# Optimization experiments

Measured on AMD Instinct MI355X. Metric: run time of the kernel, lower is better.

Reference implementation:

```python
import jax, jax.numpy as jnp
import numpy as np
import math

N = 30000; N0 = 18000; N1 = 12000; R = 5; E = 600000
H = 128; HM = 128; C = 8
L1 = 20.0; L2 = 30.0
THRESH = 0.3; THRESH_C = 1e-3
T_INNER = 20; K_OUTER = 8
EPS = 1e-5


def setup_inputs() -> dict:
    key = jax.random.key(0)
    ks = jax.random.split(key, 16)
    def w(k, shape):  # kaiming-ish fan_in init
        return jax.random.normal(k, shape, jnp.float32) / np.sqrt(shape[0])
    return {
        "feat0": jax.random.normal(ks[0], (N0, 256), jnp.float32),
        "feat1": jax.random.normal(ks[1], (N1, 128), jnp.float32),
        "W0": w(ks[2], (256, H)), "b0": jnp.zeros((H,), jnp.float32),
        "W1": w(ks[3], (128, H)), "b1": jnp.zeros((H,), jnp.float32),
        "Wm1": w(ks[4], (H, HM)), "bm1": jnp.zeros((HM,), jnp.float32),
        "Wm2": w(ks[5], (HM, HM)), "bm2": jnp.zeros((HM,), jnp.float32),
        "Wout": w(ks[6], (HM, C)), "bout": jnp.zeros((C,), jnp.float32),
        "src": jax.random.randint(ks[7], (E,), 0, N, jnp.int32),
        "dst": jax.random.randint(ks[8], (E,), 0, N, jnp.int32),
        "rel": jax.random.randint(ks[9], (E,), 0, R, jnp.int32),
    }


def _layernorm(z):
    m = z.mean(-1, keepdims=True)
    v = z.var(-1, keepdims=True)
    return (z - m) / jnp.sqrt(v + EPS)


def _forward(feat0, feat1, W0, b0, W1, b1, Wm1, bm1, Wm2, bm2, Wout, bout, src, dst, rel):
    # transfer (transf_type==2): per-type linear -> concat -> 2-layer MLP w/ layernorm
    h = jnp.concatenate([feat0 @ W0 + b0, feat1 @ W1 + b1], axis=0)   # (N, H)
    z = jax.nn.relu(_layernorm(h @ Wm1 + bm1))
    h = z @ Wm2 + bm2                                                 # (N, HM)
    # per-node standardization (torch std is unbiased, ddof=1), nan -> 0
    mu = h.mean(1, keepdims=True)
    sd = h.std(1, ddof=1, keepdims=True)
    out0 = jnp.nan_to_num((h - mu) / sd)

    # per-relation row degrees of the vertically stacked adjacency (R*N, N)
    key_e = rel * N + src                                             # (E,)
    deg = jax.ops.segment_sum(jnp.ones(E, jnp.float32), key_e, num_segments=R * N)
    safe = jnp.maximum(deg, 1.0)
    vals = jnp.where(deg > 0, 1.0 / safe, 0.0)[key_e]                 # row-normalized A weights
    dinv = jnp.where(deg > 0, 1.0 / jnp.sqrt(safe), 0.0)              # D^{-1/2}
    edge_dinv = dinv[key_e] * dinv[rel * N + dst]                     # (E,)
    active = (deg > 0).astype(jnp.float32).reshape(R, N)              # (R, N)

    def tv(x):  # relational total variation tr(X^T L_r X)/N, L_r = I - D^-1/2 A_r D^-1/2
        node_term = active @ (x * x).sum(1)                           # (R,)
        edot = (x[src] * x[dst]).sum(1)                               # (E,)
        edge_term = jax.ops.segment_sum(edge_dinv * edot, rel, num_segments=R)
        return (node_term - edge_term) / N

    ratio = 2.0 * L2 / L1
    c_l1tr = jnp.abs(tv(out0)).sum()
    u0 = jnp.full((R,), 1.0 / R, jnp.float32)

    def mirror_descent(u, w, l1tr):
        fi = l1tr + ratio
        def step(carry, t):
            u, act = carry
            T_t = jnp.sqrt(2.0 * math.log(R) / (t * fi * fi))
            u_ta = u * jnp.exp(-T_t * (ratio * u + w))
            u_new = u_ta / u_ta.sum()
            diff = jnp.sqrt(((u - u_new) ** 2).sum())
            u = jnp.where(act, u_new, u)
            return (u, act & (diff >= THRESH_C)), None
        ts = jnp.arange(1, T_INNER + 1, dtype=jnp.float32)
        (u, _), _ = jax.lax.scan(step, (u, jnp.array(True)), ts)
        return u

    def outer(carry, _):
        x, u, act = carry
        w = tv(x)
        l1tr = jnp.abs(w).sum()
        u = jnp.where(act, mirror_descent(u, w, l1tr), u)
        still = act & (l1tr / c_l1tr >= THRESH)
        ew = u[rel] * vals                                            # (E,)
        msg = jax.ops.segment_sum(ew[:, None] * x[dst], src, num_segments=N)  # (N, HM)
        x = jnp.where(still, x / (1.0 + L1) + (L1 / (1.0 + L1)) * msg, x)
        return (x, u, still), None

    (x, u, _), _ = jax.lax.scan(outer, (out0, u0, jnp.array(True)), None, length=K_OUTER)
    logits = x @ Wout + bout
    return logits, x, u


def reference(feat0, feat1, W0, b0, W1, b1, Wm1, bm1, Wm2, bm2, Wout, bout, src, dst, rel):
    return _forward(feat0, feat1, W0, b0, W1, b1, Wm1, bm1, Wm2, bm2, Wout, bout, src, dst, rel)
```

## Files before the change

kernel.cpp:

```cpp
#include <hip/hip_runtime.h>
#include <cmath>

typedef unsigned short ushort_t;
typedef unsigned int uint_t;

#define N_TOT 30000
#define N0_   18000
#define R_    5
#define E_    600000
#define RN    (R_ * N_TOT)
#define NC_   (N_TOT * 8)
#define NX_   (N_TOT * 128)
#define SCAN_NB ((RN + 1023) / 1024)

typedef __attribute__((ext_vector_type(8))) short bf16x8;
typedef __attribute__((ext_vector_type(4))) float f32x4;

__device__ __forceinline__ ushort_t f2bf(float f) {
    uint_t u = __float_as_uint(f);
    uint_t r = (u + 0x7fffu + ((u >> 16) & 1u)) >> 16;
    return (ushort_t)r;
}
__device__ __forceinline__ float bflo(uint_t v) { return __uint_as_float(v << 16); }
__device__ __forceinline__ float bfhi(uint_t v) { return __uint_as_float(v & 0xffff0000u); }

__global__ void init_kernel(float* ug, int* act) {
    if (threadIdx.x < 5) ug[threadIdx.x] = 0.2f;
    if (threadIdx.x == 0) act[0] = 1;
}

__global__ __launch_bounds__(256) void cvtfeat_kernel(const float* __restrict__ in,
                                                      ushort_t* __restrict__ out,
                                                      int nelem)
{
    int i = (blockIdx.x * 256 + threadIdx.x) * 4;
    if (i >= nelem) return;
    const float4 v = *(const float4*)(in + i);
    ushort_t o0 = f2bf(v.x), o1 = f2bf(v.y), o2 = f2bf(v.z), o3 = f2bf(v.w);
    uint_t p0 = (uint_t)o0 | ((uint_t)o1 << 16);
    uint_t p1 = (uint_t)o2 | ((uint_t)o3 << 16);
    uint2* op = (uint2*)(out + i);
    *op = make_uint2(p0, p1);
}

__global__ __launch_bounds__(256) void cvtw_kernel(const float* __restrict__ W,
                                                   ushort_t* __restrict__ wt, int K)
{
    int idx = blockIdx.x * 256 + threadIdx.x;
    if (idx >= 128 * K) return;
    int j = idx / K, k = idx - j * K;
    wt[idx] = f2bf(W[k * 128 + j]);
}

__global__ __launch_bounds__(256) void mlp_mfma_kernel(
    const ushort_t* __restrict__ fb0, const ushort_t* __restrict__ fb1,
    const ushort_t* __restrict__ wt0, const ushort_t* __restrict__ wt1,
    const ushort_t* __restrict__ wtm1, const ushort_t* __restrict__ wtm2,
    const float* __restrict__ b0, const float* __restrict__ b1,
    const float* __restrict__ bm1, const float* __restrict__ bm2,
    float* __restrict__ xout, ushort_t* __restrict__ xh)
{
    const int t = threadIdx.x;
    const int lane = t & 63;
    const int wv = t >> 6;
    const int lr = lane & 15;
    const int lg = lane >> 4;
    const int row0 = blockIdx.x * 32;

    __shared__ ushort_t hls[32][136];
    __shared__ float    tls[32][132];
    __shared__ ushort_t zls[32][136];

    #pragma unroll
    for (int mt = 0; mt < 2; ++mt) {
        const int rb = row0 + mt * 16;
        const bool is0 = (rb < N0_);
        const int r = min(rb + lr, N_TOT - 1);
        const ushort_t* __restrict__ fa =
            is0 ? fb0 + (size_t)r * 256 : fb1 + (size_t)(r - N0_) * 128;
        const ushort_t* __restrict__ wt = is0 ? wt0 : wt1;
        const int K = is0 ? 256 : 128;
        const int c0 = wv * 32 + lr;

        f32x4 a0 = {0.f, 0.f, 0.f, 0.f};
        f32x4 a1 = {0.f, 0.f, 0.f, 0.f};
        for (int ks = 0; ks < K; ks += 32) {
            const bf16x8 af = *(const bf16x8*)(fa + ks + lg * 8);
            const bf16x8 wb0 = *(const bf16x8*)(wt + (size_t)c0 * K + ks + lg * 8);
            const bf16x8 wb1 = *(const bf16x8*)(wt + (size_t)(c0 + 16) * K + ks + lg * 8);
            a0 = __builtin_amdgcn_mfma_f32_16x16x32_bf16(af, wb0, a0, 0, 0, 0);
            a1 = __builtin_amdgcn_mfma_f32_16x16x32_bf16(af, wb1, a1, 0, 0, 0);
        }
        const float bb0 = is0 ? b0[c0] : b1[c0];
        const float bb1 = is0 ? b0[c0 + 16] : b1[c0 + 16];
        #pragma unroll
        for (int j = 0; j < 4; ++j) {
            hls[mt * 16 + lg * 4 + j][c0]      = f2bf(a0[j] + bb0);
            hls[mt * 16 + lg * 4 + j][c0 + 16] = f2bf(a1[j] + bb1);
        }
    }
    __syncthreads();

    {
        const int c0 = wv * 32 + lr;
        f32x4 g00 = {0.f,0.f,0.f,0.f}, g01 = {0.f,0.f,0.f,0.f};
        f32x4 g10 = {0.f,0.f,0.f,0.f}, g11 = {0.f,0.f,0.f,0.f};
        for (int ks = 0; ks < 128; ks += 32) {
            const bf16x8 wb0 = *(const bf16x8*)(wtm1 + (size_t)c0 * 128 + ks + lg * 8);
            const bf16x8 wb1 = *(const bf16x8*)(wtm1 + (size_t)(c0 + 16) * 128 + ks + lg * 8);
            const bf16x8 af0 = *(const bf16x8*)(&hls[lr][ks + lg * 8]);
            const bf16x8 af1 = *(const bf16x8*)(&hls[16 + lr][ks + lg * 8]);
            g00 = __builtin_amdgcn_mfma_f32_16x16x32_bf16(af0, wb0, g00, 0, 0, 0);
            g01 = __builtin_amdgcn_mfma_f32_16x16x32_bf16(af0, wb1, g01, 0, 0, 0);
            g10 = __builtin_amdgcn_mfma_f32_16x16x32_bf16(af1, wb0, g10, 0, 0, 0);
            g11 = __builtin_amdgcn_mfma_f32_16x16x32_bf16(af1, wb1, g11, 0, 0, 0);
        }
        const float bb0 = bm1[c0], bb1 = bm1[c0 + 16];
        #pragma unroll
        for (int j = 0; j < 4; ++j) {
            tls[lg * 4 + j][c0]           = g00[j] + bb0;
            tls[lg * 4 + j][c0 + 16]      = g01[j] + bb1;
            tls[16 + lg * 4 + j][c0]      = g10[j] + bb0;
            tls[16 + lg * 4 + j][c0 + 16] = g11[j] + bb1;
        }
    }
    __syncthreads();

    {
        const int row = t >> 3, seg = t & 7;
        f32x4 v[4];
        float s = 0.f;
        #pragma unroll
        for (int i = 0; i < 4; ++i) {
            v[i] = *(const f32x4*)(&tls[row][seg * 16 + i * 4]);
            s += v[i][0] + v[i][1] + v[i][2] + v[i][3];
        }
        #pragma unroll
        for (int o = 1; o < 8; o <<= 1) s += __shfl_xor(s, o, 64);
        const float mean = s * (1.0f / 128.0f);
        float q = 0.f;
        #pragma unroll
        for (int i = 0; i < 4; ++i) {
            #pragma unroll
            for (int e = 0; e < 4; ++e) { float d = v[i][e] - mean; q = fmaf(d, d, q); }
        }
        #pragma unroll
        for (int o = 1; o < 8; o <<= 1) q += __shfl_xor(q, o, 64);
        const float inv = 1.0f / sqrtf(q * (1.0f / 128.0f) + 1e-5f);
        uint_t* zp = (uint_t*)&zls[row][0];
        #pragma unroll
        for (int i = 0; i < 4; ++i) {
            ushort_t z0 = f2bf(fmaxf((v[i][0] - mean) * inv, 0.0f));
            ushort_t z1 = f2bf(fmaxf((v[i][1] - mean) * inv, 0.0f));
            ushort_t z2 = f2bf(fmaxf((v[i][2] - mean) * inv, 0.0f));
            ushort_t z3 = f2bf(fmaxf((v[i][3] - mean) * inv, 0.0f));
            zp[(seg * 16 + i * 4) / 2]     = (uint_t)z0 | ((uint_t)z1 << 16);
            zp[(seg * 16 + i * 4) / 2 + 1] = (uint_t)z2 | ((uint_t)z3 << 16);
        }
    }
    __syncthreads();

    {
        const int c0 = wv * 32 + lr;
        f32x4 g00 = {0.f,0.f,0.f,0.f}, g01 = {0.f,0.f,0.f,0.f};
        f32x4 g10 = {0.f,0.f,0.f,0.f}, g11 = {0.f,0.f,0.f,0.f};
        for (int ks = 0; ks < 128; ks += 32) {
            const bf16x8 wb0 = *(const bf16x8*)(wtm2 + (size_t)c0 * 128 + ks + lg * 8);
            const bf16x8 wb1 = *(const bf16x8*)(wtm2 + (size_t)(c0 + 16) * 128 + ks + lg * 8);
            const bf16x8 af0 = *(const bf16x8*)(&zls[lr][ks + lg * 8]);
            const bf16x8 af1 = *(const bf16x8*)(&zls[16 + lr][ks + lg * 8]);
            g00 = __builtin_amdgcn_mfma_f32_16x16x32_bf16(af0, wb0, g00, 0, 0, 0);
            g01 = __builtin_amdgcn_mfma_f32_16x16x32_bf16(af0, wb1, g01, 0, 0, 0);
            g10 = __builtin_amdgcn_mfma_f32_16x16x32_bf16(af1, wb0, g10, 0, 0, 0);
            g11 = __builtin_amdgcn_mfma_f32_16x16x32_bf16(af1, wb1, g11, 0, 0, 0);
        }
        __syncthreads();
        const float bb0 = bm2[c0], bb1 = bm2[c0 + 16];
        #pragma unroll
        for (int j = 0; j < 4; ++j) {
            tls[lg * 4 + j][c0]           = g00[j] + bb0;
            tls[lg * 4 + j][c0 + 16]      = g01[j] + bb1;
            tls[16 + lg * 4 + j][c0]      = g10[j] + bb0;
            tls[16 + lg * 4 + j][c0 + 16] = g11[j] + bb1;
        }
    }
    __syncthreads();

    {
        const int row = t >> 3, seg = t & 7;
        const int n = row0 + row;
        f32x4 v[4];
        float s = 0.f;
        #pragma unroll
        for (int i = 0; i < 4; ++i) {
            v[i] = *(const f32x4*)(&tls[row][seg * 16 + i * 4]);
            s += v[i][0] + v[i][1] + v[i][2] + v[i][3];
        }
        #pragma unroll
        for (int o = 1; o < 8; o <<= 1) s += __shfl_xor(s, o, 64);
        const float mu = s * (1.0f / 128.0f);
        float q = 0.f;
        #pragma unroll
        for (int i = 0; i < 4; ++i) {
            #pragma unroll
            for (int e = 0; e < 4; ++e) { float d = v[i][e] - mu; q = fmaf(d, d, q); }
        }
        #pragma unroll
        for (int o = 1; o < 8; o <<= 1) q += __shfl_xor(q, o, 64);
        const float sd = sqrtf(q * (1.0f / 127.0f));
        const float inv = 1.0f / sd;
        if (n < N_TOT) {
            uint_t* xhp = (uint_t*)xh + (size_t)n * 64 + seg * 8;
            float* xop = xout + (size_t)n * 128 + seg * 16;
            #pragma unroll
            for (int i = 0; i < 4; ++i) {
                float rr[4];
                #pragma unroll
                for (int e = 0; e < 4; ++e) {
                    float r = (v[i][e] - mu) * inv;
                    if (!(fabsf(r) <= 3.402823466e38f)) {
                        r = (r != r) ? 0.0f : ((r > 0.0f) ? 3.402823466e38f : -3.402823466e38f);
                    }
                    rr[e] = r;
                }
                *(float4*)(xop + i * 4) = make_float4(rr[0], rr[1], rr[2], rr[3]);
                xhp[i * 2]     = (uint_t)f2bf(rr[0]) | ((uint_t)f2bf(rr[1]) << 16);
                xhp[i * 2 + 1] = (uint_t)f2bf(rr[2]) | ((uint_t)f2bf(rr[3]) << 16);
            }
        }
    }
}

__global__ void deg_kernel(const int* __restrict__ src, const int* __restrict__ rel,
                           int* __restrict__ deg_i)
{
    int e = blockIdx.x * 256 + threadIdx.x;
    if (e >= E_) return;
    atomicAdd(&deg_i[rel[e] * N_TOT + src[e]], 1);
}

__global__ void dinv_kernel(const int* __restrict__ deg_i, float* __restrict__ dinv)
{
    int i = blockIdx.x * 256 + threadIdx.x;
    if (i >= RN) return;
    int dg = deg_i[i];
    dinv[i] = (dg > 0) ? 1.0f / sqrtf((float)dg) : 0.0f;
}

__global__ __launch_bounds__(256) void scan1_kernel(const int* __restrict__ cnt,
                                                    int* __restrict__ rp,
                                                    int* __restrict__ bsum)
{
    __shared__ int wsum[4];
    const int t = threadIdx.x, lane = t & 63, w = t >> 6;
    const int i0 = blockIdx.x * 1024 + t * 4;
    const int v0 = (i0 + 0 < RN) ? cnt[i0 + 0] : 0;
    const int v1 = (i0 + 1 < RN) ? cnt[i0 + 1] : 0;
    const int v2 = (i0 + 2 < RN) ? cnt[i0 + 2] : 0;
    const int v3 = (i0 + 3 < RN) ? cnt[i0 + 3] : 0;
    const int s = v0 + v1 + v2 + v3;
    int sc = s;
    #pragma unroll
    for (int o = 1; o < 64; o <<= 1) { int tmp = __shfl_up(sc, o, 64); if (lane >= o) sc += tmp; }
    if (lane == 63) wsum[w] = sc;
    __syncthreads();
    int woff = 0;
    #pragma unroll
    for (int i = 0; i < 3; ++i) if (i < w) woff += wsum[i];
    int run = woff + sc - s;
    if (i0 + 0 < RN) rp[i0 + 0] = run; run += v0;
    if (i0 + 1 < RN) rp[i0 + 1] = run; run += v1;
    if (i0 + 2 < RN) rp[i0 + 2] = run; run += v2;
    if (i0 + 3 < RN) rp[i0 + 3] = run;
    if (t == 255) bsum[blockIdx.x] = woff + sc;
}

__global__ __launch_bounds__(256) void scan2_kernel(const int* __restrict__ bsum,
                                                    int* __restrict__ boff,
                                                    int* __restrict__ rp)
{
    __shared__ int wsum[4];
    const int t = threadIdx.x, lane = t & 63, w = t >> 6;
    const int v = (t < SCAN_NB) ? bsum[t] : 0;
    int sc = v;
    #pragma unroll
    for (int o = 1; o < 64; o <<= 1) { int tmp = __shfl_up(sc, o, 64); if (lane >= o) sc += tmp; }
    if (lane == 63) wsum[w] = sc;
    __syncthreads();
    int woff = 0;
    #pragma unroll
    for (int i = 0; i < 3; ++i) if (i < w) woff += wsum[i];
    boff[t] = woff + sc - v;
    if (t == 0) rp[RN] = E_;
}

__global__ __launch_bounds__(256) void scan3_kernel(int* __restrict__ rp,
                                                    const int* __restrict__ boff)
{
    const int off = boff[blockIdx.x];
    if (off == 0) return;
    const int i0 = blockIdx.x * 1024 + threadIdx.x * 4;
    if (i0 + 3 < RN) {
        int4* p = (int4*)(rp + i0);
        int4 q = *p;
        q.x += off; q.y += off; q.z += off; q.w += off;
        *p = q;
    } else {
        for (int i = 0; i < 4; ++i)
            if (i0 + i < RN) rp[i0 + i] += off;
    }
}

__global__ void scatter_kernel(const int* __restrict__ src, const int* __restrict__ dst,
                               const int* __restrict__ rel, const int* __restrict__ rp,
                               int* __restrict__ fill, const int* __restrict__ deg_i,
                               const float* __restrict__ dinv,
                               int* __restrict__ csr_dst, float* __restrict__ csr_w,
                               float* __restrict__ csr_edinv)
{
    int e = blockIdx.x * 256 + threadIdx.x;
    if (e >= E_) return;
    int s = src[e], r = rel[e], d = dst[e];
    int key = r * N_TOT + s;
    int pos = rp[key] + atomicAdd(&fill[key], 1);
    csr_dst[pos] = d;
    csr_w[pos] = 1.0f / (float)deg_i[key];
    csr_edinv[pos] = dinv[key] * dinv[r * N_TOT + d];
}

__global__ __launch_bounds__(256) void tv_kernel(
    const ushort_t* __restrict__ xh, const int* __restrict__ rp,
    const int* __restrict__ csr_dst, const float* __restrict__ csr_edinv,
    const int* __restrict__ act, int k, float* __restrict__ accbuf)
{
    if (act[k] == 0) return;
    const int lane = threadIdx.x & 63;
    const int wv = threadIdx.x >> 6;
    const int wid = blockIdx.x * 4 + wv;
    const int nw = gridDim.x * 4;
    float na[5] = {0, 0, 0, 0, 0};
    float ea[5] = {0, 0, 0, 0, 0};
    for (int n = wid; n < N_TOT; n += nw) {
        const uint_t vs = ((const uint_t*)(xh + (size_t)n * 128))[lane];
        const float sx = bflo(vs), sy = bfhi(vs);
        const float pp = fmaf(sx, sx, sy * sy);
        #pragma unroll
        for (int r = 0; r < 5; ++r) {
            const int e0 = rp[r * N_TOT + n];
            const int e1 = rp[r * N_TOT + n + 1];
            if (e1 > e0) na[r] += pp;
            float acc0 = 0.0f, acc1 = 0.0f;
            int e = e0;
            for (; e + 2 <= e1; e += 2) {
                const int dn0 = csr_dst[e];
                const int dn1 = csr_dst[e + 1];
                const float w0 = csr_edinv[e];
                const float w1 = csr_edinv[e + 1];
                const uint_t v0 = ((const uint_t*)(xh + (size_t)dn0 * 128))[lane];
                const uint_t v1 = ((const uint_t*)(xh + (size_t)dn1 * 128))[lane];
                acc0 = fmaf(w0, fmaf(sx, bflo(v0), sy * bfhi(v0)), acc0);
                acc1 = fmaf(w1, fmaf(sx, bflo(v1), sy * bfhi(v1)), acc1);
            }
            if (e < e1) {
                const int dn0 = csr_dst[e];
                const float w0 = csr_edinv[e];
                const uint_t v0 = ((const uint_t*)(xh + (size_t)dn0 * 128))[lane];
                acc0 = fmaf(w0, fmaf(sx, bflo(v0), sy * bfhi(v0)), acc0);
            }
            ea[r] += acc0 + acc1;
        }
    }
    __shared__ float sacc[4][10];
    #pragma unroll
    for (int r = 0; r < 5; ++r) {
        float a = na[r], b2 = ea[r];
        for (int o = 32; o > 0; o >>= 1) {
            a += __shfl_down(a, o, 64);
            b2 += __shfl_down(b2, o, 64);
        }
        if (lane == 0) { sacc[wv][r] = a; sacc[wv][5 + r] = b2; }
    }
    __syncthreads();
    if (threadIdx.x < 10) {
        float t = sacc[0][threadIdx.x] + sacc[1][threadIdx.x] +
                  sacc[2][threadIdx.x] + sacc[3][threadIdx.x];
        atomicAdd(&accbuf[k * 16 + threadIdx.x], t);
    }
}

__global__ void scalar_kernel(const float* __restrict__ accbuf, float* __restrict__ ug,
                              float* __restrict__ c_l1, int* __restrict__ act, int k)
{
    if (blockIdx.x != 0 || threadIdx.x >= 8) return;
    const int r = threadIdx.x;
    const int a = act[k];
    float w = (r < 5) ? (accbuf[k * 16 + r] - accbuf[k * 16 + 5 + r]) * (1.0f / 30000.0f)
                      : 0.0f;
    float l1 = fabsf(w);
    for (int o = 4; o > 0; o >>= 1) l1 += __shfl_xor(l1, o, 8);
    if (k == 0 && r == 0) c_l1[0] = l1;
    if (!a) { if (r == 0) act[k + 1] = 0; return; }
    float u = (r < 5) ? ug[r] : 0.0f;
    const float fi = l1 + 3.0f;
    bool mact = true;
    for (int t = 1; t <= 20; ++t) {
        float T = sqrtf(3.2188758248682006f / ((float)t * fi * fi));
        float ta = u * expf(-T * (3.0f * u + w));
        float ssum = ta;
        for (int o = 4; o > 0; o >>= 1) ssum += __shfl_xor(ssum, o, 8);
        float un = ta / ssum;
        float d0 = u - un;
        float dq = d0 * d0;
        for (int o = 4; o > 0; o >>= 1) dq += __shfl_xor(dq, o, 8);
        if (mact) u = un;
        mact = mact && (sqrtf(dq) >= 1e-3f);
    }
    if (r < 5) ug[r] = u;
    if (r == 0) act[k + 1] = (l1 / c_l1[0] >= 0.3f) ? 1 : 0;
}

__global__ __launch_bounds__(256) void msg_upd_kernel(
    float* __restrict__ x, const ushort_t* __restrict__ xh_in,
    ushort_t* __restrict__ xh_out,
    const int* __restrict__ rp, const int* __restrict__ csr_dst,
    const float* __restrict__ csr_w, const float* __restrict__ ug,
    const int* __restrict__ act, int k)
{
    if (act[k + 1] == 0) return;
    const int lane = threadIdx.x & 63;
    const int wid = blockIdx.x * 4 + (threadIdx.x >> 6);
    const int nw = gridDim.x * 4;
    const float u0 = ug[0], u1 = ug[1], u2 = ug[2], u3 = ug[3], u4 = ug[4];
    for (int n = wid; n < N_TOT; n += nw) {
        float ax0 = 0.0f, ay0 = 0.0f, ax1 = 0.0f, ay1 = 0.0f;
        #pragma unroll
        for (int r = 0; r < 5; ++r) {
            const float ur = (r == 0) ? u0 : (r == 1) ? u1 : (r == 2) ? u2 : (r == 3) ? u3 : u4;
            const int e0 = rp[r * N_TOT + n];
            const int e1 = rp[r * N_TOT + n + 1];
            int e = e0;
            for (; e + 2 <= e1; e += 2) {
                const float w0 = ur * csr_w[e];
                const float w1 = ur * csr_w[e + 1];
                const int dn0 = csr_dst[e];
                const int dn1 = csr_dst[e + 1];
                const uint_t v0 = ((const uint_t*)(xh_in + (size_t)dn0 * 128))[lane];
                const uint_t v1 = ((const uint_t*)(xh_in + (size_t)dn1 * 128))[lane];
                ax0 = fmaf(w0, bflo(v0), ax0);
                ay0 = fmaf(w0, bfhi(v0), ay0);
                ax1 = fmaf(w1, bflo(v1), ax1);
                ay1 = fmaf(w1, bfhi(v1), ay1);
            }
            if (e < e1) {
                const float w0 = ur * csr_w[e];
                const int dn0 = csr_dst[e];
                const uint_t v0 = ((const uint_t*)(xh_in + (size_t)dn0 * 128))[lane];
                ax0 = fmaf(w0, bflo(v0), ax0);
                ay0 = fmaf(w0, bfhi(v0), ay0);
            }
        }
        const float ci = 1.0f / 21.0f, cb = 20.0f / 21.0f;
        float2* xp = (float2*)(x + (size_t)n * 128);
        const float2 xs = xp[lane];
        const float nx_ = fmaf(cb, ax0 + ax1, xs.x * ci);
        const float ny_ = fmaf(cb, ay0 + ay1, xs.y * ci);
        xp[lane] = make_float2(nx_, ny_);
        ((uint_t*)(xh_out + (size_t)n * 128))[lane] =
            ((uint_t)f2bf(ny_) << 16) | (uint_t)f2bf(nx_);
    }
}

__global__ __launch_bounds__(256) void final_kernel(const float* __restrict__ x,
                                                    const float* __restrict__ Wout,
                                                    const float* __restrict__ bout,
                                                    const float* __restrict__ ug,
                                                    float* __restrict__ out)
{
    const int nl = threadIdx.x >> 7;
    const int n = blockIdx.x * 2 + nl;
    const int j = threadIdx.x & 127;
    const int lane = threadIdx.x & 63;
    const int wv = threadIdx.x >> 6;
    float xv = x[(size_t)n * 128 + j];
    out[(size_t)NC_ + (size_t)n * 128 + j] = xv;
    float p[8];
    #pragma unroll
    for (int c = 0; c < 8; ++c) p[c] = xv * Wout[j * 8 + c];
    #pragma unroll
    for (int c = 0; c < 8; ++c)
        for (int o = 32; o > 0; o >>= 1) p[c] += __shfl_down(p[c], o, 64);
    __shared__ float sp[4][8];
    if (lane == 0) {
        #pragma unroll
        for (int c = 0; c < 8; ++c) sp[wv][c] = p[c];
    }
    __syncthreads();
    if (j < 8) {
        int c = j;
        out[(size_t)n * 8 + c] = bout[c] + sp[2 * nl][c] + sp[2 * nl + 1][c];
    }
    if (blockIdx.x == 0 && threadIdx.x < 5)
        out[(size_t)NC_ + (size_t)NX_ + threadIdx.x] = ug[threadIdx.x];
}

extern "C" void kernel_launch(void* const* d_in, const int* in_sizes, int n_in,
                              void* d_out, int out_size, void* d_ws, size_t ws_size,
                              hipStream_t stream)
{
    const float* feat0 = (const float*)d_in[0];
    const float* feat1 = (const float*)d_in[1];
    const float* W0   = (const float*)d_in[2];
    const float* b0   = (const float*)d_in[3];
    const float* W1   = (const float*)d_in[4];
    const float* b1   = (const float*)d_in[5];
    const float* Wm1  = (const float*)d_in[6];
    const float* bm1  = (const float*)d_in[7];
    const float* Wm2  = (const float*)d_in[8];
    const float* bm2  = (const float*)d_in[9];
    const float* Wout = (const float*)d_in[10];
    const float* bout = (const float*)d_in[11];
    const int* src = (const int*)d_in[12];
    const int* dst = (const int*)d_in[13];
    const int* rel = (const int*)d_in[14];
    float* out = (float*)d_out;

    char* p = (char*)d_ws;
    auto alloc = [&](size_t bytes) { char* q = p; p += (bytes + 255) & ~(size_t)255; return q; };
    float*    xbuf      = (float*)   alloc((size_t)NX_ * 4);
    ushort_t* xh0       = (ushort_t*)alloc((size_t)NX_ * 2);
    ushort_t* xh1       = (ushort_t*)alloc((size_t)NX_ * 2);
    ushort_t* fb0       = (ushort_t*)alloc((size_t)N0_ * 256 * 2);
    ushort_t* fb1       = (ushort_t*)alloc((size_t)(N_TOT - N0_) * 128 * 2);
    ushort_t* wt0       = (ushort_t*)alloc((size_t)128 * 256 * 2);
    ushort_t* wt1       = (ushort_t*)alloc((size_t)128 * 128 * 2);
    ushort_t* wtm1      = (ushort_t*)alloc((size_t)128 * 128 * 2);
    ushort_t* wtm2      = (ushort_t*)alloc((size_t)128 * 128 * 2);
    int*      deg_i     = (int*)     alloc((size_t)RN * 4);
    float*    dinv      = (float*)   alloc((size_t)RN * 4);
    int*      rp        = (int*)     alloc(((size_t)RN + 1) * 4);
    int*      fill      = (int*)     alloc((size_t)RN * 4);
    int*      bsum      = (int*)     alloc((size_t)SCAN_NB * 4);
    int*      boff      = (int*)     alloc(256 * 4);
    int*      csr_dst   = (int*)     alloc((size_t)E_ * 4);
    float*    csr_w     = (float*)   alloc((size_t)E_ * 4);
    float*    csr_edinv = (float*)   alloc((size_t)E_ * 4);
    float*    accbuf    = (float*)   alloc(128 * 4);
    float*    ug        = (float*)   alloc(64);
    float*    c_l1      = (float*)   alloc(64);
    int*      act       = (int*)     alloc(64);

    hipMemsetAsync(deg_i, 0, (size_t)RN * 4, stream);
    hipMemsetAsync(fill, 0, (size_t)RN * 4, stream);
    hipMemsetAsync(accbuf, 0, 128 * 4, stream);
    init_kernel<<<1, 64, 0, stream>>>(ug, act);

    cvtfeat_kernel<<<(N0_ * 256 / 4 + 255) / 256, 256, 0, stream>>>(feat0, fb0, N0_ * 256);
    cvtfeat_kernel<<<((N_TOT - N0_) * 128 / 4 + 255) / 256, 256, 0, stream>>>(
        feat1, fb1, (N_TOT - N0_) * 128);
    cvtw_kernel<<<(128 * 256 + 255) / 256, 256, 0, stream>>>(W0, wt0, 256);
    cvtw_kernel<<<(128 * 128 + 255) / 256, 256, 0, stream>>>(W1, wt1, 128);
    cvtw_kernel<<<(128 * 128 + 255) / 256, 256, 0, stream>>>(Wm1, wtm1, 128);
    cvtw_kernel<<<(128 * 128 + 255) / 256, 256, 0, stream>>>(Wm2, wtm2, 128);

    mlp_mfma_kernel<<<(N_TOT + 31) / 32, 256, 0, stream>>>(
        fb0, fb1, wt0, wt1, wtm1, wtm2, b0, b1, bm1, bm2, xbuf, xh0);

    deg_kernel<<<(E_ + 255) / 256, 256, 0, stream>>>(src, rel, deg_i);
    dinv_kernel<<<(RN + 255) / 256, 256, 0, stream>>>(deg_i, dinv);
    scan1_kernel<<<SCAN_NB, 256, 0, stream>>>(deg_i, rp, bsum);
    scan2_kernel<<<1, 256, 0, stream>>>(bsum, boff, rp);
    scan3_kernel<<<SCAN_NB, 256, 0, stream>>>(rp, boff);
    scatter_kernel<<<(E_ + 255) / 256, 256, 0, stream>>>(src, dst, rel, rp, fill,
                                                         deg_i, dinv,
                                                         csr_dst, csr_w, csr_edinv);

    ushort_t* ha = xh0;
    ushort_t* hb = xh1;
    for (int k = 0; k < 8; ++k) {
        tv_kernel<<<2048, 256, 0, stream>>>(ha, rp, csr_dst, csr_edinv, act, k, accbuf);
        scalar_kernel<<<1, 64, 0, stream>>>(accbuf, ug, c_l1, act, k);
        msg_upd_kernel<<<2048, 256, 0, stream>>>(xbuf, ha, hb, rp, csr_dst, csr_w,
                                                 ug, act, k);
        ushort_t* t = ha; ha = hb; hb = t;
    }

    final_kernel<<<N_TOT / 2, 256, 0, stream>>>(xbuf, Wout, bout, ug, out);
}
```

Before: 470.9 us.

## Switch CSR to node-major relation layout and merge per-relation edge loops

Reorders the degree/row-pointer key from relation-major to node-major so each node's edges across all relations are contiguous. The TV and message-update kernels then walk one merged edge range per node, 4-way unrolled, and derive each edge's relation by comparing against the boundaries. Row pointers are read as wave-uniform scalars. This removes five short per-relation loops with remainder tails and raises in-flight gathers, at the cost of extra compare/select work per edge.

```diff
diff --git a/kernel.cpp b/kernel.cpp
--- a/kernel.cpp
+++ b/kernel.cpp
@@ -236,7 +236,7 @@
 {
     int e = blockIdx.x * 256 + threadIdx.x;
     if (e >= E_) return;
-    atomicAdd(&deg_i[rel[e] * N_TOT + src[e]], 1);
+    atomicAdd(&deg_i[src[e] * R_ + rel[e]], 1);
 }
 
 __global__ void dinv_kernel(const int* __restrict__ deg_i, float* __restrict__ dinv)
@@ -321,11 +321,11 @@
     int e = blockIdx.x * 256 + threadIdx.x;
     if (e >= E_) return;
     int s = src[e], r = rel[e], d = dst[e];
-    int key = r * N_TOT + s;
+    int key = s * R_ + r;
     int pos = rp[key] + atomicAdd(&fill[key], 1);
     csr_dst[pos] = d;
     csr_w[pos] = 1.0f / (float)deg_i[key];
-    csr_edinv[pos] = dinv[key] * dinv[r * N_TOT + d];
+    csr_edinv[pos] = dinv[key] * dinv[d * R_ + r];
 }
 
 __global__ __launch_bounds__(256) void tv_kernel(
@@ -341,44 +341,68 @@
     float na[5] = {0, 0, 0, 0, 0};
     float ea[5] = {0, 0, 0, 0, 0};
     for (int n = wid; n < N_TOT; n += nw) {
+        const int b0 = __builtin_amdgcn_readfirstlane(rp[n * R_ + 0]);
+        const int b1 = __builtin_amdgcn_readfirstlane(rp[n * R_ + 1]);
+        const int b2 = __builtin_amdgcn_readfirstlane(rp[n * R_ + 2]);
+        const int b3 = __builtin_amdgcn_readfirstlane(rp[n * R_ + 3]);
+        const int b4 = __builtin_amdgcn_readfirstlane(rp[n * R_ + 4]);
+        const int b5 = __builtin_amdgcn_readfirstlane(rp[n * R_ + 5]);
         const uint_t vs = ((const uint_t*)(xh + (size_t)n * 128))[lane];
         const float sx = bflo(vs), sy = bfhi(vs);
         const float pp = fmaf(sx, sx, sy * sy);
-        #pragma unroll
-        for (int r = 0; r < 5; ++r) {
-            const int e0 = rp[r * N_TOT + n];
-            const int e1 = rp[r * N_TOT + n + 1];
-            if (e1 > e0) na[r] += pp;
-            float acc0 = 0.0f, acc1 = 0.0f;
-            int e = e0;
-            for (; e + 2 <= e1; e += 2) {
-                const int dn0 = csr_dst[e];
-                const int dn1 = csr_dst[e + 1];
-                const float w0 = csr_edinv[e];
-                const float w1 = csr_edinv[e + 1];
-                const uint_t v0 = ((const uint_t*)(xh + (size_t)dn0 * 128))[lane];
-                const uint_t v1 = ((const uint_t*)(xh + (size_t)dn1 * 128))[lane];
-                acc0 = fmaf(w0, fmaf(sx, bflo(v0), sy * bfhi(v0)), acc0);
-                acc1 = fmaf(w1, fmaf(sx, bflo(v1), sy * bfhi(v1)), acc1);
+        if (b1 > b0) na[0] += pp;
+        if (b2 > b1) na[1] += pp;
+        if (b3 > b2) na[2] += pp;
+        if (b4 > b3) na[3] += pp;
+        if (b5 > b4) na[4] += pp;
+        int e = b0;
+        for (; e + 4 <= b5; e += 4) {
+            const int dn0 = csr_dst[e + 0];
+            const int dn1 = csr_dst[e + 1];
+            const int dn2 = csr_dst[e + 2];
+            const int dn3 = csr_dst[e + 3];
+            const float w0 = csr_edinv[e + 0];
+            const float w1 = csr_edinv[e + 1];
+            const float w2 = csr_edinv[e + 2];
+            const float w3 = csr_edinv[e + 3];
+            const uint_t v0 = ((const uint_t*)(xh + (size_t)dn0 * 128))[lane];
+            const uint_t v1 = ((const uint_t*)(xh + (size_t)dn1 * 128))[lane];
+            const uint_t v2 = ((const uint_t*)(xh + (size_t)dn2 * 128))[lane];
+            const uint_t v3 = ((const uint_t*)(xh + (size_t)dn3 * 128))[lane];
+            const float d0 = w0 * fmaf(sx, bflo(v0), sy * bfhi(v0));
+            const float d1 = w1 * fmaf(sx, bflo(v1), sy * bfhi(v1));
+            const float d2 = w2 * fmaf(sx, bflo(v2), sy * bfhi(v2));
+            const float d3 = w3 * fmaf(sx, bflo(v3), sy * bfhi(v3));
+            const int r0 = (e + 0 >= b1) + (e + 0 >= b2) + (e + 0 >= b3) + (e + 0 >= b4);
+            const int r1 = (e + 1 >= b1) + (e + 1 >= b2) + (e + 1 >= b3) + (e + 1 >= b4);
+            const int r2 = (e + 2 >= b1) + (e + 2 >= b2) + (e + 2 >= b3) + (e + 2 >= b4);
+            const int r3 = (e + 3 >= b1) + (e + 3 >= b2) + (e + 3 >= b3) + (e + 3 >= b4);
+            #pragma unroll
+            for (int rr = 0; rr < 5; ++rr) {
+                ea[rr] += (r0 == rr ? d0 : 0.0f) + (r1 == rr ? d1 : 0.0f) +
+                          (r2 == rr ? d2 : 0.0f) + (r3 == rr ? d3 : 0.0f);
             }
-            if (e < e1) {
-                const int dn0 = csr_dst[e];
-                const float w0 = csr_edinv[e];
-                const uint_t v0 = ((const uint_t*)(xh + (size_t)dn0 * 128))[lane];
-                acc0 = fmaf(w0, fmaf(sx, bflo(v0), sy * bfhi(v0)), acc0);
-            }
-            ea[r] += acc0 + acc1;
+        }
+        for (; e < b5; ++e) {
+            const int dn0 = csr_dst[e];
+            const float w0 = csr_edinv[e];
+            const uint_t v0 = ((const uint_t*)(xh + (size_t)dn0 * 128))[lane];
+            const float d0 = w0 * fmaf(sx, bflo(v0), sy * bfhi(v0));
+            const int r0 = (e >= b1) + (e >= b2) + (e >= b3) + (e >= b4);
+            #pragma unroll
+            for (int rr = 0; rr < 5; ++rr)
+                ea[rr] += (r0 == rr ? d0 : 0.0f);
         }
     }
     __shared__ float sacc[4][10];
     #pragma unroll
     for (int r = 0; r < 5; ++r) {
-        float a = na[r], b2 = ea[r];
+        float a = na[r], b = ea[r];
         for (int o = 32; o > 0; o >>= 1) {
             a += __shfl_down(a, o, 64);
-            b2 += __shfl_down(b2, o, 64);
-        }
-        if (lane == 0) { sacc[wv][r] = a; sacc[wv][5 + r] = b2; }
+            b += __shfl_down(b, o, 64);
+        }
+        if (lane == 0) { sacc[wv][r] = a; sacc[wv][5 + r] = b; }
     }
     __syncthreads();
     if (threadIdx.x < 10) {
@@ -432,32 +456,48 @@
     const int nw = gridDim.x * 4;
     const float u0 = ug[0], u1 = ug[1], u2 = ug[2], u3 = ug[3], u4 = ug[4];
     for (int n = wid; n < N_TOT; n += nw) {
+        const int b1 = __builtin_amdgcn_readfirstlane(rp[n * R_ + 1]);
+        const int b2 = __builtin_amdgcn_readfirstlane(rp[n * R_ + 2]);
+        const int b3 = __builtin_amdgcn_readfirstlane(rp[n * R_ + 3]);
+        const int b4 = __builtin_amdgcn_readfirstlane(rp[n * R_ + 4]);
+        const int b0 = __builtin_amdgcn_readfirstlane(rp[n * R_ + 0]);
+        const int b5 = __builtin_amdgcn_readfirstlane(rp[n * R_ + 5]);
         float ax0 = 0.0f, ay0 = 0.0f, ax1 = 0.0f, ay1 = 0.0f;
-        #pragma unroll
-        for (int r = 0; r < 5; ++r) {
-            const float ur = (r == 0) ? u0 : (r == 1) ? u1 : (r == 2) ? u2 : (r == 3) ? u3 : u4;
-            const int e0 = rp[r * N_TOT + n];
-            const int e1 = rp[r * N_TOT + n + 1];
-            int e = e0;
-            for (; e + 2 <= e1; e += 2) {
-                const float w0 = ur * csr_w[e];
-                const float w1 = ur * csr_w[e + 1];
-                const int dn0 = csr_dst[e];
-                const int dn1 = csr_dst[e + 1];
-                const uint_t v0 = ((const uint_t*)(xh_in + (size_t)dn0 * 128))[lane];
-                const uint_t v1 = ((const uint_t*)(xh_in + (size_t)dn1 * 128))[lane];
-                ax0 = fmaf(w0, bflo(v0), ax0);
-                ay0 = fmaf(w0, bfhi(v0), ay0);
-                ax1 = fmaf(w1, bflo(v1), ax1);
-                ay1 = fmaf(w1, bfhi(v1), ay1);
-            }
-            if (e < e1) {
-                const float w0 = ur * csr_w[e];
-                const int dn0 = csr_dst[e];
-                const uint_t v0 = ((const uint_t*)(xh_in + (size_t)dn0 * 128))[lane];
-                ax0 = fmaf(w0, bflo(v0), ax0);
-                ay0 = fmaf(w0, bfhi(v0), ay0);
-            }
+        int e = b0;
+        for (; e + 4 <= b5; e += 4) {
+            const int r0 = (e + 0 >= b1) + (e + 0 >= b2) + (e + 0 >= b3) + (e + 0 >= b4);
+            const int r1 = (e + 1 >= b1) + (e + 1 >= b2) + (e + 1 >= b3) + (e + 1 >= b4);
+            const int r2 = (e + 2 >= b1) + (e + 2 >= b2) + (e + 2 >= b3) + (e + 2 >= b4);
+            const int r3 = (e + 3 >= b1) + (e + 3 >= b2) + (e + 3 >= b3) + (e + 3 >= b4);
+            const float uu0 = (r0 == 0) ? u0 : (r0 == 1) ? u1 : (r0 == 2) ? u2 : (r0 == 3) ? u3 : u4;
+            const float uu1 = (r1 == 0) ? u0 : (r1 == 1) ? u1 : (r1 == 2) ? u2 : (r1 == 3) ? u3 : u4;
+            const float uu2 = (r2 == 0) ? u0 : (r2 == 1) ? u1 : (r2 == 2) ? u2 : (r2 == 3) ? u3 : u4;
+            const float uu3 = (r3 == 0) ? u0 : (r3 == 1) ? u1 : (r3 == 2) ? u2 : (r3 == 3) ? u3 : u4;
+            const int dn0 = csr_dst[e + 0];
+            const int dn1 = csr_dst[e + 1];
+            const int dn2 = csr_dst[e + 2];
+            const int dn3 = csr_dst[e + 3];
+            const float w0 = uu0 * csr_w[e + 0];
+            const float w1 = uu1 * csr_w[e + 1];
+            const float w2 = uu2 * csr_w[e + 2];
+            const float w3 = uu3 * csr_w[e + 3];
+            const uint_t v0 = ((const uint_t*)(xh_in + (size_t)dn0 * 128))[lane];
+            const uint_t v1 = ((const uint_t*)(xh_in + (size_t)dn1 * 128))[lane];
+            const uint_t v2 = ((const uint_t*)(xh_in + (size_t)dn2 * 128))[lane];
+            const uint_t v3 = ((const uint_t*)(xh_in + (size_t)dn3 * 128))[lane];
+            ax0 = fmaf(w0, bflo(v0), ax0); ay0 = fmaf(w0, bfhi(v0), ay0);
+            ax1 = fmaf(w1, bflo(v1), ax1); ay1 = fmaf(w1, bfhi(v1), ay1);
+            ax0 = fmaf(w2, bflo(v2), ax0); ay0 = fmaf(w2, bfhi(v2), ay0);
+            ax1 = fmaf(w3, bflo(v3), ax1); ay1 = fmaf(w3, bfhi(v3), ay1);
+        }
+        for (; e < b5; ++e) {
+            const int r0 = (e >= b1) + (e >= b2) + (e >= b3) + (e >= b4);
+            const float uu0 = (r0 == 0) ? u0 : (r0 == 1) ? u1 : (r0 == 2) ? u2 : (r0 == 3) ? u3 : u4;
+            const int dn0 = csr_dst[e];
+            const float w0 = uu0 * csr_w[e];
+            const uint_t v0 = ((const uint_t*)(xh_in + (size_t)dn0 * 128))[lane];
+            ax0 = fmaf(w0, bflo(v0), ax0);
+            ay0 = fmaf(w0, bfhi(v0), ay0);
         }
         const float ci = 1.0f / 21.0f, cb = 20.0f / 21.0f;
         float2* xp = (float2*)(x + (size_t)n * 128);
```

New measurement: 445.2 us. -5.5%, faster.
